# Performance work log

Hardware: AMD Instinct MI355X
Metric: run time of the kernel (lower is better)

## Reference

```python
import jax, jax.numpy as jnp
import numpy as np

NUM_OBJ_CLS = 151  # VG object classes incl. background
C = NUM_OBJ_CLS - 1  # multi-hot width = 150
PATH_DIM = 1024
B, P = 128, 512  # images, pairs per image


def setup_inputs() -> dict:
    key = jax.random.key(0)
    k1, k2, k3 = jax.random.split(key, 3)
    # predicted object-class labels per image; foreground classes 1..150
    pair_preds = jax.random.randint(k1, (B, P), 1, NUM_OBJ_CLS)
    W = jax.random.normal(k2, (PATH_DIM, C), dtype=jnp.float32) * 0.02
    b = jax.random.normal(k3, (PATH_DIM,), dtype=jnp.float32) * 0.02
    return {"pair_preds": pair_preds, "W": W, "b": b}


def reference(pair_preds, W, b):
    # Per image, build a multi-hot over the 150 foreground classes:
    # tmp[:, p-1] = 1 for every predicted label p (set is idempotent, so
    # the np.unique in the original is immaterial). Every row of an image
    # shares the same multi-hot vector.
    Bq, Pq = pair_preds.shape
    cols = pair_preds - 1  # [B, P]
    multi_hot = jnp.zeros((Bq, C), dtype=jnp.float32)
    multi_hot = multi_hot.at[jnp.arange(Bq)[:, None], cols].set(1.0)  # [B, C]
    # Each image contributes pairs.shape[0] = P identical rows, concatenated.
    context = jnp.repeat(multi_hot, Pq, axis=0)  # [B*P, C]
    # Linear projection: [B*P, C] @ [C, D] + [D]
    return context @ W.T + b
```

## Files before the change

### kernel.cpp

```cpp
#include <hip/hip_runtime.h>

#define NB   128
#define NP   512
#define NC   150
#define ND   1024
#define BROWS 32
#define BCHUNKS (NP / BROWS)

typedef float  f4 __attribute__((ext_vector_type(4)));
typedef float  f2 __attribute__((ext_vector_type(2)));
typedef int    i4 __attribute__((ext_vector_type(4)));

__global__ __launch_bounds__(256) void compute_y_kernel(const int* __restrict__ preds,
                                                        const float* __restrict__ W,
                                                        const float* __restrict__ bias,
                                                        float* __restrict__ out) {
    __shared__ float sflag[NC];
    const unsigned bid  = blockIdx.x;
    const unsigned img  = bid >> 2;
    const unsigned dblk = bid & 3;
    const unsigned t    = threadIdx.x;

    if (t < NC) sflag[t] = 0.0f;
    __syncthreads();

    if (t < NP / 4) {
        i4 c4 = ((const i4*)(preds + (size_t)img * NP))[t];
        sflag[c4.x - 1] = 1.0f;
        sflag[c4.y - 1] = 1.0f;
        sflag[c4.z - 1] = 1.0f;
        sflag[c4.w - 1] = 1.0f;
    }
    __syncthreads();

    const int d = (int)(dblk * 256 + t);
    const f2* w = (const f2*)(W + (size_t)d * NC);
    float y = bias[d];
    #pragma unroll 5
    for (int j = 0; j < NC / 2; ++j) {
        const f2 a = w[j];
        y += sflag[2 * j] * a.x + sflag[2 * j + 1] * a.y;
    }
    out[(size_t)img * NP * ND + (size_t)d] = y;
}

__global__ __launch_bounds__(256) void broadcast_kernel(const f4* __restrict__ src,
                                                        f4* __restrict__ out) {
    const unsigned bid   = blockIdx.x;
    const unsigned img   = bid >> 4;
    const unsigned chunk = bid & 15;
    const unsigned t     = threadIdx.x;

    const size_t base = ((size_t)img << 17);
    const f4 v = src[base + t];

    unsigned p0 = chunk * BROWS;
    if (chunk == 0) p0 = 1;
    const unsigned p1 = chunk * BROWS + BROWS;

    #pragma unroll 4
    for (unsigned p = p0; p < p1; ++p) {
        out[base + ((size_t)p << 8) + t] = v;
    }
}

extern "C" void kernel_launch(void* const* d_in, const int* in_sizes, int n_in,
                              void* d_out, int out_size, void* d_ws, size_t ws_size,
                              hipStream_t stream) {
    const int*   preds = (const int*)d_in[0];
    const float* W     = (const float*)d_in[1];
    const float* bias  = (const float*)d_in[2];
    float*       out   = (float*)d_out;

    compute_y_kernel<<<dim3(NB * 4), dim3(256), 0, stream>>>(preds, W, bias, out);
    broadcast_kernel<<<dim3(NB * BCHUNKS), dim3(256), 0, stream>>>((const f4*)out, (f4*)out);
}
```

Baseline: 56.10 us.

## Stage W tiles in LDS and split the class reduction across four thread groups

Result: no change. 55.89 us (-0.4%).

```diff
diff --git a/kernel.cpp b/kernel.cpp
--- a/kernel.cpp
+++ b/kernel.cpp
@@ -4,28 +4,42 @@
 #define NP   512
 #define NC   150
 #define ND   1024
+#define AD   64
+#define ADB  (ND / AD)
 #define BROWS 32
 #define BCHUNKS (NP / BROWS)
 
 typedef float  f4 __attribute__((ext_vector_type(4)));
-typedef float  f2 __attribute__((ext_vector_type(2)));
 typedef int    i4 __attribute__((ext_vector_type(4)));
 
 __global__ __launch_bounds__(256) void compute_y_kernel(const int* __restrict__ preds,
                                                         const float* __restrict__ W,
                                                         const float* __restrict__ bias,
                                                         float* __restrict__ out) {
+    __shared__ float wl[AD * NC];
     __shared__ float sflag[NC];
+    __shared__ float part[4][AD];
+
     const unsigned bid  = blockIdx.x;
-    const unsigned img  = bid >> 2;
-    const unsigned dblk = bid & 3;
+    const unsigned img  = bid >> 4;
+    const unsigned dblk = bid & 15;
     const unsigned t    = threadIdx.x;
 
+    i4 c4;
+    if (t < NP / 4) c4 = ((const i4*)(preds + (size_t)img * NP))[t];
+
     if (t < NC) sflag[t] = 0.0f;
+
+    const f4* wsrc = (const f4*)(W + (size_t)dblk * AD * NC);
+    f4* wdst = (f4*)wl;
+    #pragma unroll
+    for (int i = 0; i < 10; ++i) {
+        unsigned g = i * 256u + t;
+        if (g < (AD * NC) / 4) wdst[g] = wsrc[g];
+    }
     __syncthreads();
 
     if (t < NP / 4) {
-        i4 c4 = ((const i4*)(preds + (size_t)img * NP))[t];
         sflag[c4.x - 1] = 1.0f;
         sflag[c4.y - 1] = 1.0f;
         sflag[c4.z - 1] = 1.0f;
@@ -33,15 +47,23 @@
     }
     __syncthreads();
 
-    const int d = (int)(dblk * 256 + t);
-    const f2* w = (const f2*)(W + (size_t)d * NC);
-    float y = bias[d];
-    #pragma unroll 5
-    for (int j = 0; j < NC / 2; ++j) {
-        const f2 a = w[j];
-        y += sflag[2 * j] * a.x + sflag[2 * j + 1] * a.y;
+    const unsigned d = t & 63;
+    const unsigned q = t >> 6;
+    const unsigned c0 = q * 38;
+    const unsigned c1 = (q == 3) ? NC : c0 + 38;
+    float acc = 0.0f;
+    const float* wrow = wl + (size_t)d * NC;
+    for (unsigned c = c0; c < c1; ++c) {
+        acc += sflag[c] * wrow[c];
     }
-    out[(size_t)img * NP * ND + (size_t)d] = y;
+    part[q][d] = acc;
+    __syncthreads();
+
+    if (t < AD) {
+        const unsigned dg = dblk * AD + t;
+        float y = bias[dg] + part[0][t] + part[1][t] + part[2][t] + part[3][t];
+        out[(size_t)img * NP * ND + dg] = y;
+    }
 }
 
 __global__ __launch_bounds__(256) void broadcast_kernel(const f4* __restrict__ src,
@@ -72,6 +94,6 @@
     const float* bias  = (const float*)d_in[2];
     float*       out   = (float*)d_out;
 
-    compute_y_kernel<<<dim3(NB * 4), dim3(256), 0, stream>>>(preds, W, bias, out);
+    compute_y_kernel<<<dim3(NB * ADB), dim3(256), 0, stream>>>(preds, W, bias, out);
     broadcast_kernel<<<dim3(NB * BCHUNKS), dim3(256), 0, stream>>>((const f4*)out, (f4*)out);
 }
```

## Fuse compute and broadcast into a single kernel writing rows from LDS

Applied to the files above, without the earlier changes.

Result: faster. 52.47 us (-6.5%).

```diff
diff --git a/kernel.cpp b/kernel.cpp
--- a/kernel.cpp
+++ b/kernel.cpp
@@ -4,28 +4,30 @@
 #define NP   512
 #define NC   150
 #define ND   1024
-#define BROWS 32
-#define BCHUNKS (NP / BROWS)
 
 typedef float  f4 __attribute__((ext_vector_type(4)));
 typedef float  f2 __attribute__((ext_vector_type(2)));
 typedef int    i4 __attribute__((ext_vector_type(4)));
 
-__global__ __launch_bounds__(256) void compute_y_kernel(const int* __restrict__ preds,
-                                                        const float* __restrict__ W,
-                                                        const float* __restrict__ bias,
-                                                        float* __restrict__ out) {
+__global__ __launch_bounds__(256) void labellayer_onepass(const int* __restrict__ preds,
+                                                          const float* __restrict__ W,
+                                                          const float* __restrict__ bias,
+                                                          float* __restrict__ out) {
     __shared__ float sflag[NC];
+    __shared__ float ys[256];
+
     const unsigned bid  = blockIdx.x;
     const unsigned img  = bid >> 2;
     const unsigned dblk = bid & 3;
     const unsigned t    = threadIdx.x;
 
+    i4 c4;
+    if (t < NP / 4) c4 = ((const i4*)(preds + (size_t)img * NP))[t];
+
     if (t < NC) sflag[t] = 0.0f;
     __syncthreads();
 
     if (t < NP / 4) {
-        i4 c4 = ((const i4*)(preds + (size_t)img * NP))[t];
         sflag[c4.x - 1] = 1.0f;
         sflag[c4.y - 1] = 1.0f;
         sflag[c4.z - 1] = 1.0f;
@@ -33,7 +35,7 @@
     }
     __syncthreads();
 
-    const int d = (int)(dblk * 256 + t);
+    const unsigned d = dblk * 256u + t;
     const f2* w = (const f2*)(W + (size_t)d * NC);
     float y = bias[d];
     #pragma unroll 5
@@ -41,26 +43,18 @@
         const f2 a = w[j];
         y += sflag[2 * j] * a.x + sflag[2 * j + 1] * a.y;
     }
-    out[(size_t)img * NP * ND + (size_t)d] = y;
-}
+    ys[t] = y;
+    __syncthreads();
 
-__global__ __launch_bounds__(256) void broadcast_kernel(const f4* __restrict__ src,
-                                                        f4* __restrict__ out) {
-    const unsigned bid   = blockIdx.x;
-    const unsigned img   = bid >> 4;
-    const unsigned chunk = bid & 15;
-    const unsigned t     = threadIdx.x;
+    const unsigned wv = t >> 6;
+    const unsigned ln = t & 63;
+    const f4 v = ((const f4*)ys)[ln];
 
-    const size_t base = ((size_t)img << 17);
-    const f4 v = src[base + t];
-
-    unsigned p0 = chunk * BROWS;
-    if (chunk == 0) p0 = 1;
-    const unsigned p1 = chunk * BROWS + BROWS;
-
-    #pragma unroll 4
-    for (unsigned p = p0; p < p1; ++p) {
-        out[base + ((size_t)p << 8) + t] = v;
+    f4* o = (f4*)out + ((size_t)img << 17)
+                     + (size_t)dblk * 64 + ln;
+    #pragma unroll 8
+    for (unsigned p = wv; p < NP; p += 4) {
+        o[(size_t)p << 8] = v;
     }
 }
 
@@ -72,6 +66,5 @@
     const float* bias  = (const float*)d_in[2];
     float*       out   = (float*)d_out;
 
-    compute_y_kernel<<<dim3(NB * 4), dim3(256), 0, stream>>>(preds, W, bias, out);
-    broadcast_kernel<<<dim3(NB * BCHUNKS), dim3(256), 0, stream>>>((const f4*)out, (f4*)out);
+    labellayer_onepass<<<dim3(NB * 4), dim3(256), 0, stream>>>(preds, W, bias, out);
 }
```
